# Performance work log

Measured on AMD Instinct MI355X. Metric: run time of the kernel, lower is better.

## Reference

```python
import jax, jax.numpy as jnp
import numpy as np

# --- low precision float format: exp=5, man=2, subnormals, nearest-even ---
EXP, MAN = 5, 2
BIAS = 2 ** (EXP - 1) - 1          # 15
EMIN = 1 - BIAS                     # -14 (min normal exponent; clamping here gives subnormals)
MAXV = (2.0 - 2.0 ** (-MAN)) * 2.0 ** BIAS


def _q(x):
    """Round x to nearest FP(exp=5, man=2) value (subnormals, clipped at max)."""
    ax = jnp.abs(x)
    e = jnp.floor(jnp.log2(jnp.where(ax > 0, ax, 1.0)))
    e = jnp.maximum(e, EMIN)
    scale = jnp.exp2(e - MAN)
    q = jnp.round(x / scale) * scale   # jnp.round = half-to-even
    q = jnp.clip(q, -MAXV, MAXV)
    return jnp.where(ax > 0, q, x).astype(x.dtype)


# Quantizer: forward quantize, straight-through (quantized) backward
@jax.custom_vjp
def fq(x):
    return _q(x)

def _fq_fwd(x):
    return _q(x), None

def _fq_bwd(_, g):
    return (_q(g),)

fq.defvjp(_fq_fwd, _fq_bwd)


def conv_valid(x, w):
    return jax.lax.conv_general_dilated(
        x, w, window_strides=(1, 1), padding='VALID',
        dimension_numbers=('NCHW', 'OIHW', 'NCHW'))


def qconv(x, w):
    # QConv2d: input_quant, weight_quant, conv, output_quant
    return fq(conv_valid(fq(x), fq(w)))


def qlinear(x, W, b):
    # QLinear: input_quant, weight_quant (weights + bias), matmul, output_quant
    return fq(fq(x) @ fq(W).T + fq(b))


def batchnorm(x, gamma, beta, eps=1e-5):
    # training-mode BatchNorm2d over (N,H,W) per channel
    m = x.mean(axis=(0, 2, 3), keepdims=True)
    v = x.var(axis=(0, 2, 3), keepdims=True)
    return (x - m) * jax.lax.rsqrt(v + eps) * gamma[None, :, None, None] + beta[None, :, None, None]


def maxpool2(x):
    return jax.lax.reduce_window(x, -jnp.inf, jax.lax.max,
                                 (1, 1, 2, 2), (1, 1, 2, 2), 'VALID')


def setup_inputs() -> dict:
    key = jax.random.key(0)
    ks = jax.random.split(key, 12)
    B = 8192
    inp = {
        'x':   jax.random.normal(ks[0], (B, 1, 32, 32), jnp.float32),
        'w1':  jax.random.normal(ks[1], (6, 1, 5, 5), jnp.float32) * 0.2,
        'g1':  jnp.ones((6,), jnp.float32),
        'be1': jnp.zeros((6,), jnp.float32),
        'w2':  jax.random.normal(ks[2], (16, 6, 5, 5), jnp.float32) * 0.1,
        'g2':  jnp.ones((16,), jnp.float32),
        'be2': jnp.zeros((16,), jnp.float32),
        'fw1': jax.random.normal(ks[3], (120, 400), jnp.float32) * 0.05,
        'fb1': jnp.zeros((120,), jnp.float32),
        'fw2': jax.random.normal(ks[4], (84, 120), jnp.float32) * 0.09,
        'fb2': jnp.zeros((84,), jnp.float32),
        'fw3': jax.random.normal(ks[5], (10, 84), jnp.float32) * 0.1,
        'fb3': jnp.zeros((10,), jnp.float32),
    }
    return inp


def reference(x, w1, g1, be1, w2, g2, be2, fw1, fb1, fw2, fb2, fw3, fb3):
    x = fq(x)                                   # act_error_quant
    x = qconv(x, w1)                            # conv1 (no bias)
    x = batchnorm(x, g1, be1)                   # bn1
    x = fq(x)                                   # act_error_quant
    x = maxpool2(jax.nn.relu(x))                # relu + 2x2 maxpool -> [B,6,14,14]
    x = qconv(x, w2)                            # conv2 -> [B,16,10,10]
    x = batchnorm(x, g2, be2)                   # bn2
    x = fq(x)
    x = maxpool2(jax.nn.relu(x))                # -> [B,16,5,5]
    x = x.reshape(x.shape[0], -1)               # [B,400]
    x = jax.nn.relu(qlinear(x, fw1, fb1))       # fc1
    x = jax.nn.relu(qlinear(x, fw2, fb2))       # fc2
    x = qlinear(x, fw3, fb3)                    # fc3 -> [B,10]
    return x
```

## Files before the change

kernel.cpp:

```cpp
#include <hip/hip_runtime.h>
#include <hip/hip_bf16.h>


#define BATCH 8192

__device__ __forceinline__ double fq_d(double x) {
    long long b = __double_as_longlong(x);
    long long ab = b & 0x7fffffffffffffffLL;
    if (ab == 0) return x;
    double q;
    if (ab >= 0x3F10000000000000LL) {
        long long r = b + 0x0001FFFFFFFFFFFFLL + ((b >> 50) & 1LL);
        r &= 0xFFFC000000000000LL;
        q = __longlong_as_double(r);
        q = fmin(fmax(q, -57344.0), 57344.0);
    } else {
        q = rint(x * 65536.0) * 1.52587890625e-05;
    }
    return q;
}

__device__ __forceinline__ unsigned short bfbits(double q) {
    __hip_bfloat16 h = __float2bfloat16((float)q);
    return *(unsigned short*)&h;
}

__global__ void kprep(const float* __restrict__ w1, const float* __restrict__ w2,
                      const float* __restrict__ fb1, const float* __restrict__ fb2,
                      const float* __restrict__ fb3, const float* __restrict__ fw1,
                      const float* __restrict__ fw2, const float* __restrict__ fw3,
                      float* __restrict__ qw1, float* __restrict__ qw2,
                      float* __restrict__ qfb1, float* __restrict__ qfb2,
                      float* __restrict__ qfb3, float* __restrict__ Wt1,
                      float* __restrict__ Wt2, float* __restrict__ Wt3) {
    int i = blockIdx.x * 256 + threadIdx.x;
    if (i < 150) { qw1[i] = (float)fq_d((double)w1[i]); return; }
    i -= 150;
    if (i < 2400) { qw2[i] = (float)fq_d((double)w2[i]); return; }
    i -= 2400;
    if (i < 120) { qfb1[i] = (float)fq_d((double)fb1[i]); return; }
    i -= 120;
    if (i < 84) { qfb2[i] = (float)fq_d((double)fb2[i]); return; }
    i -= 84;
    if (i < 10) { qfb3[i] = (float)fq_d((double)fb3[i]); return; }
    i -= 10;
    if (i < 51200) { int k = i / 128, o = i % 128;
        Wt1[i] = (o < 120) ? (float)fq_d((double)fw1[o * 400 + k]) : 0.0f; return; }
    i -= 51200;
    if (i < 15360) { int k = i / 128, o = i % 128;
        Wt2[i] = (o < 84) ? (float)fq_d((double)fw2[o * 120 + k]) : 0.0f; return; }
    i -= 15360;
    if (i < 1344) { int k = i / 16, o = i % 16;
        Wt3[i] = (o < 10) ? (float)fq_d((double)fw3[o * 84 + k]) : 0.0f; return; }
}
#define PREP_TOTAL (150 + 2400 + 120 + 84 + 10 + 51200 + 15360 + 1344)

__global__ __launch_bounds__(256) void kconv1(const float* __restrict__ x,
        const float* __restrict__ qw, __hip_bfloat16* __restrict__ c1,
        int nimg_total, double* __restrict__ st1) {
    __shared__ float sxf[3 * 1056];
    __shared__ double swd[152];
    __shared__ double sred[6][2];
    int t = threadIdx.x;
    int b0 = blockIdx.x * 3;
    int nimg = nimg_total - b0; if (nimg > 3) nimg = 3;
    for (int i = t; i < nimg * 1024; i += 256) {
        int img = i >> 10, idx = i & 1023;
        sxf[img * 1056 + (idx >> 5) * 33 + (idx & 31)] =
            (float)fq_d((double)x[(size_t)(b0 + img) * 1024 + idx]);
    }
    if (t < 150) swd[t] = (double)qw[t];
    if (t >= 192 && t < 204) ((double*)sred)[t - 192] = 0.0;
    __syncthreads();
    int ntask = nimg * 336;
    for (int task = t; task < ntask; task += 256) {
        int img = task / 336; int rr = task % 336;
        int co = rr / 56; int rem = rr % 56;
        int i0 = (rem >> 2) * 2;
        int j0 = (rem & 3) * 7;
        const float* xb = &sxf[img * 1056];
        const double* wp = &swd[co * 25];
        double a0[7], a1[7];
        #pragma unroll
        for (int j = 0; j < 7; ++j) { a0[j] = 0.0; a1[j] = 0.0; }
        double wr[5], wq[5];
        #pragma unroll
        for (int u = 0; u < 6; ++u) {
            const float* xr = &sxf[img * 1056 + (i0 + u) * 33 + j0];
            double xv[11];
            #pragma unroll
            for (int k = 0; k < 11; ++k) xv[k] = (double)xr[k];
            if (u < 5) {
                #pragma unroll
                for (int tt = 0; tt < 5; ++tt) wr[tt] = wp[u * 5 + tt];
                #pragma unroll
                for (int j = 0; j < 7; ++j)
                    a0[j] = fma(xv[j], wr[0], fma(xv[j+1], wr[1], fma(xv[j+2], wr[2],
                            fma(xv[j+3], wr[3], fma(xv[j+4], wr[4], a0[j])))));
            }
            if (u >= 1) {
                #pragma unroll
                for (int j = 0; j < 7; ++j)
                    a1[j] = fma(xv[j], wq[0], fma(xv[j+1], wq[1], fma(xv[j+2], wq[2],
                            fma(xv[j+3], wq[3], fma(xv[j+4], wq[4], a1[j])))));
            }
            #pragma unroll
            for (int tt = 0; tt < 5; ++tt) wq[tt] = wr[tt];
        }
        size_t base = ((size_t)(b0 + img) * 6 + co) * 784 + (size_t)i0 * 28 + j0;
        double s = 0.0, s2 = 0.0;
        #pragma unroll
        for (int j = 0; j < 7; ++j) {
            double q0 = fq_d(a0[j]), q1 = fq_d(a1[j]);
            ((unsigned short*)c1)[base + j]      = bfbits(q0);
            ((unsigned short*)c1)[base + 28 + j] = bfbits(q1);
            s += q0 + q1; s2 += q0 * q0 + q1 * q1;
        }
        atomicAdd(&sred[co][0], s);
        atomicAdd(&sred[co][1], s2);
    }
    __syncthreads();
    if (t < 12) atomicAdd(&st1[t * 32 + (blockIdx.x & 31)], ((double*)sred)[t]);
}

__global__ void kfinal(const double* __restrict__ st, double* __restrict__ mr,
                       int C, double N) {
    int c = threadIdx.x;
    if (c < C) {
        double s = 0.0, s2 = 0.0;
        for (int b = 0; b < 32; ++b) { s += st[c * 64 + b]; s2 += st[c * 64 + 32 + b]; }
        double m = s / N;
        double v = s2 / N - m * m;
        mr[2 * c] = m;
        mr[2 * c + 1] = 1.0 / sqrt(v + 1e-5);
    }
}

__global__ __launch_bounds__(256) void kpool1(const __hip_bfloat16* __restrict__ c1,
        const double* __restrict__ mr1, const float* __restrict__ g1,
        const float* __restrict__ be1, __hip_bfloat16* __restrict__ p1) {
    int idx = blockIdx.x * 256 + threadIdx.x;
    int pp = idx % 7;  int t1 = idx / 7;
    int ph = t1 % 14;  int t2 = t1 / 14;
    int c  = t2 % 6;   int b  = t2 / 6;
    double m = mr1[2 * c], r = mr1[2 * c + 1];
    double gg = (double)g1[c], bb = (double)be1[c];
    bool useMax = (r * gg) >= 0.0;
    const __hip_bfloat16* src = c1 + (((size_t)b * 6 + c) * 28 + 2 * ph) * 28 + 4 * pp;
    ushort4 u0 = *(const ushort4*)src;
    ushort4 u1 = *(const ushort4*)(src + 28);
    float f0 = __bfloat162float(*(__hip_bfloat16*)&u0.x), f1 = __bfloat162float(*(__hip_bfloat16*)&u0.y);
    float f2 = __bfloat162float(*(__hip_bfloat16*)&u0.z), f3 = __bfloat162float(*(__hip_bfloat16*)&u0.w);
    float f4 = __bfloat162float(*(__hip_bfloat16*)&u1.x), f5 = __bfloat162float(*(__hip_bfloat16*)&u1.y);
    float f6 = __bfloat162float(*(__hip_bfloat16*)&u1.z), f7 = __bfloat162float(*(__hip_bfloat16*)&u1.w);
    float va = useMax ? fmaxf(fmaxf(f0, f1), fmaxf(f4, f5))
                      : fminf(fminf(f0, f1), fminf(f4, f5));
    float vb = useMax ? fmaxf(fmaxf(f2, f3), fmaxf(f6, f7))
                      : fminf(fminf(f2, f3), fminf(f6, f7));
    double qa = fq_d((((double)va - m) * r) * gg + bb);
    double qb = fq_d((((double)vb - m) * r) * gg + bb);
    qa = fmax(qa, 0.0); qb = fmax(qb, 0.0);
    ushort2 pk; pk.x = bfbits(qa); pk.y = bfbits(qb);
    *(ushort2*)&p1[((size_t)b * 6 + c) * 196 + ph * 14 + 2 * pp] = pk;
}

__global__ __launch_bounds__(320) void kconv2(const __hip_bfloat16* __restrict__ p1,
        const float* __restrict__ qw, __hip_bfloat16* __restrict__ c2,
        double* __restrict__ st2) {
    __shared__ float sxf[4704];
    __shared__ float swf[2400];
    __shared__ double sred[16][2];
    int t = threadIdx.x;
    int b0 = blockIdx.x * 4;
    for (int i = t; i < 4704; i += 320) sxf[i] = __bfloat162float(p1[(size_t)b0 * 1176 + i]);
    for (int i = t; i < 2400; i += 320) swf[i] = qw[i];
    if (t < 32) ((double*)sred)[t] = 0.0;
    __syncthreads();
    int img = t / 80, r = t % 80;
    int co = r / 5, i0 = (r % 5) * 2;
    const float* xb = &sxf[img * 1176];
    const float* wb = &swf[co * 150];
    double a0[10], a1[10];
    #pragma unroll
    for (int j = 0; j < 10; ++j) { a0[j] = 0.0; a1[j] = 0.0; }
    double wr[5], wq[5];
    for (int ci = 0; ci < 6; ++ci) {
        #pragma unroll
        for (int u = 0; u < 6; ++u) {
            const float* xr = &xb[ci * 196 + (i0 + u) * 14];
            double xv[14];
            #pragma unroll
            for (int k = 0; k < 14; ++k) xv[k] = (double)xr[k];
            if (u < 5) {
                #pragma unroll
                for (int tt = 0; tt < 5; ++tt) wr[tt] = (double)wb[ci * 25 + u * 5 + tt];
                #pragma unroll
                for (int j = 0; j < 10; ++j)
                    a0[j] = fma(xv[j], wr[0], fma(xv[j+1], wr[1], fma(xv[j+2], wr[2],
                            fma(xv[j+3], wr[3], fma(xv[j+4], wr[4], a0[j])))));
            }
            if (u >= 1) {
                #pragma unroll
                for (int j = 0; j < 10; ++j)
                    a1[j] = fma(xv[j], wq[0], fma(xv[j+1], wq[1], fma(xv[j+2], wq[2],
                            fma(xv[j+3], wq[3], fma(xv[j+4], wq[4], a1[j])))));
            }
            #pragma unroll
            for (int tt = 0; tt < 5; ++tt) wq[tt] = wr[tt];
        }
    }
    size_t base = ((size_t)(b0 + img) * 16 + co) * 100 + (size_t)i0 * 10;
    double s = 0.0, s2 = 0.0;
    #pragma unroll
    for (int j = 0; j < 10; ++j) {
        double q0 = fq_d(a0[j]), q1 = fq_d(a1[j]);
        ((unsigned short*)c2)[base + j]      = bfbits(q0);
        ((unsigned short*)c2)[base + 10 + j] = bfbits(q1);
        s += q0 + q1; s2 += q0 * q0 + q1 * q1;
    }
    atomicAdd(&sred[co][0], s);
    atomicAdd(&sred[co][1], s2);
    __syncthreads();
    if (t < 32) atomicAdd(&st2[t * 32 + (blockIdx.x & 31)], ((double*)sred)[t]);
}

__global__ __launch_bounds__(256) void kfc1(const __hip_bfloat16* __restrict__ c2,
        const double* __restrict__ mr2, const float* __restrict__ g2,
        const float* __restrict__ be2, const float* __restrict__ Wt,
        const float* __restrict__ qb, __hip_bfloat16* __restrict__ outb) {
    constexpr int IN = 400, OUT = 120, OUTP = 128, ROWS = 8, BT = 16;
    __shared__ double sx[BT][IN];
    __shared__ double sbn[16][4];
    int t = threadIdx.x;
    int b0 = blockIdx.x * BT;
    if (t < 16) {
        sbn[t][0] = mr2[2 * t]; sbn[t][1] = mr2[2 * t + 1];
        sbn[t][2] = (double)g2[t]; sbn[t][3] = (double)be2[t];
    }
    __syncthreads();
    for (int i = t; i < BT * IN; i += 256) {
        int r = i / IN, k = i % IN;
        int c = k / 25, rem = k % 25;
        int ph = rem / 5, pw = rem % 5;
        const __hip_bfloat16* src = c2 + (((size_t)(b0 + r) * 16 + c) * 10 + 2 * ph) * 10 + 2 * pw;
        double m = sbn[c][0], rr = sbn[c][1], gg = sbn[c][2], bb = sbn[c][3];
        float f0 = __bfloat162float(src[0]),  f1 = __bfloat162float(src[1]);
        float f2 = __bfloat162float(src[10]), f3 = __bfloat162float(src[11]);
        bool useMax = (rr * gg) >= 0.0;
        float v = useMax ? fmaxf(fmaxf(f0, f1), fmaxf(f2, f3))
                         : fminf(fminf(f0, f1), fminf(f2, f3));
        double q = fq_d((((double)v - m) * rr) * gg + bb);
        sx[r][k] = fmax(q, 0.0);
    }
    __syncthreads();
    int o = t % OUTP;
    int g = t / OUTP;
    double acc[ROWS];
    double bias = (o < OUT) ? (double)qb[o] : 0.0;
    #pragma unroll
    for (int r = 0; r < ROWS; ++r) acc[r] = bias;
    #pragma unroll 4
    for (int k = 0; k < IN; ++k) {
        double w = (double)Wt[k * OUTP + o];
        #pragma unroll
        for (int r = 0; r < ROWS; ++r)
            acc[r] = fma(sx[g * ROWS + r][k], w, acc[r]);
    }
    if (o < OUT) {
        #pragma unroll
        for (int r = 0; r < ROWS; ++r) {
            double q = fq_d(acc[r]);
            if (q < 0.0) q = 0.0;
            outb[(size_t)(b0 + g * ROWS + r) * OUT + o] = __float2bfloat16((float)q);
        }
    }
}

template<int IN, int OUT, int OUTP, int ROWS>
__global__ __launch_bounds__(256) void kfc(const __hip_bfloat16* __restrict__ X,
        const float* __restrict__ Wt, const float* __restrict__ qb,
        __hip_bfloat16* __restrict__ outb, float* __restrict__ outf, int do_relu) {
    constexpr int GROUPS = 256 / OUTP;
    constexpr int BT = ROWS * GROUPS;
    __shared__ double sx[BT][IN];
    int t = threadIdx.x;
    int b0 = blockIdx.x * BT;
    for (int i = t; i < BT * IN; i += 256) {
        int r = i / IN, k = i % IN;
        sx[r][k] = (double)__bfloat162float(X[(size_t)(b0 + r) * IN + k]);
    }
    __syncthreads();
    int o = t % OUTP;
    int g = t / OUTP;
    double acc[ROWS];
    double bias = (o < OUT) ? (double)qb[o] : 0.0;
    #pragma unroll
    for (int r = 0; r < ROWS; ++r) acc[r] = bias;
    #pragma unroll 4
    for (int k = 0; k < IN; ++k) {
        double w = (double)Wt[k * OUTP + o];
        #pragma unroll
        for (int r = 0; r < ROWS; ++r)
            acc[r] = fma(sx[g * ROWS + r][k], w, acc[r]);
    }
    if (o < OUT) {
        #pragma unroll
        for (int r = 0; r < ROWS; ++r) {
            double q = fq_d(acc[r]);
            if (do_relu && q < 0.0) q = 0.0;
            size_t b = (size_t)(b0 + g * ROWS + r);
            if (outf) outf[b * OUT + o] = (float)q;
            else      outb[b * OUT + o] = __float2bfloat16((float)q);
        }
    }
}

extern "C" void kernel_launch(void* const* d_in, const int* in_sizes, int n_in,
                              void* d_out, int out_size, void* d_ws, size_t ws_size,
                              hipStream_t stream) {
    const float* x   = (const float*)d_in[0];
    const float* w1  = (const float*)d_in[1];
    const float* g1  = (const float*)d_in[2];
    const float* be1 = (const float*)d_in[3];
    const float* w2  = (const float*)d_in[4];
    const float* g2  = (const float*)d_in[5];
    const float* be2 = (const float*)d_in[6];
    const float* fw1 = (const float*)d_in[7];
    const float* fb1 = (const float*)d_in[8];
    const float* fw2 = (const float*)d_in[9];
    const float* fb2 = (const float*)d_in[10];
    const float* fw3 = (const float*)d_in[11];
    const float* fb3 = (const float*)d_in[12];

    char* ws = (char*)d_ws;
    double* stats1 = (double*)(ws + 0);
    double* stats2 = (double*)(ws + 3072);
    double* mr1    = (double*)(ws + 11264);
    double* mr2    = (double*)(ws + 11392);
    float* qw1  = (float*)(ws + 12288);
    float* qw2  = (float*)(ws + 13312);
    float* qfb1 = (float*)(ws + 23040);
    float* qfb2 = (float*)(ws + 23552);
    float* qfb3 = (float*)(ws + 24064);
    float* Wt1  = (float*)(ws + 24576);
    float* Wt2  = (float*)(ws + 229376);
    float* Wt3  = (float*)(ws + 290816);
    __hip_bfloat16* c1 = (__hip_bfloat16*)(ws + 303104);
    __hip_bfloat16* p1 = (__hip_bfloat16*)(ws + 77373440);
    __hip_bfloat16* c2 = (__hip_bfloat16*)(ws + 303104);
    __hip_bfloat16* a1 = (__hip_bfloat16*)(ws + 303104 + 26214400);
    __hip_bfloat16* a2 = (__hip_bfloat16*)(ws + 303104 + 28180480);

    hipMemsetAsync(ws, 0, 11264, stream);

    kprep<<<(PREP_TOTAL + 255) / 256, 256, 0, stream>>>(
        w1, w2, fb1, fb2, fb3, fw1, fw2, fw3,
        qw1, qw2, qfb1, qfb2, qfb3, Wt1, Wt2, Wt3);

    kconv1<<<(BATCH + 2) / 3, 256, 0, stream>>>(x, qw1, c1, BATCH, stats1);
    kfinal<<<1, 32, 0, stream>>>(stats1, mr1, 6, (double)BATCH * 784.0);
    kpool1<<<BATCH * 6 * 14 * 7 / 256, 256, 0, stream>>>(c1, mr1, g1, be1, p1);
    kconv2<<<BATCH / 4, 320, 0, stream>>>(p1, qw2, c2, stats2);
    kfinal<<<1, 32, 0, stream>>>(stats2, mr2, 16, (double)BATCH * 100.0);
    kfc1<<<BATCH / 16, 256, 0, stream>>>(c2, mr2, g2, be2, Wt1, qfb1, a1);
    kfc<120, 84, 128, 8><<<BATCH / 16, 256, 0, stream>>>(a1, Wt2, qfb2, a2, (float*)nullptr, 1);
    kfc<84, 10, 16, 1><<<BATCH / 16, 256, 0, stream>>>(a2, Wt3, qfb3, (__hip_bfloat16*)nullptr, (float*)d_out, 0);
}
```

Baseline: 436.4 us.

## Fuse fc2/fc3, fold BN2 finalize into fc1, use float quantizer

Merges the fc2 and fc3 kernels into one kernel that keeps the fc2 activations in shared memory, which removes the a2 round trip through global memory. It also drops the second kfinal launch by having each kfc1 block reduce the conv2 statistics itself, and halves the fc1 tile so twice as many blocks run. A float-precision quantizer replaces the double one for input and weight quantization. The trade-offs are redundant statistic reductions in every fc1 block and a possible rounding difference between the float and double quantizer paths.

```diff
diff --git a/kernel.cpp b/kernel.cpp
--- a/kernel.cpp
+++ b/kernel.cpp
@@ -20,6 +20,22 @@
     return q;
 }
 
+__device__ __forceinline__ float fq_f(float x) {
+    int b = __float_as_int(x);
+    int ab = b & 0x7fffffff;
+    if (ab == 0) return x;
+    float q;
+    if (ab >= 0x38800000) {
+        int r = b + 0x000FFFFF + ((b >> 21) & 1);
+        r &= 0xFFE00000;
+        q = __int_as_float(r);
+        q = fminf(fmaxf(q, -57344.0f), 57344.0f);
+    } else {
+        q = rintf(x * 65536.0f) * 1.52587890625e-05f;
+    }
+    return q;
+}
+
 __device__ __forceinline__ unsigned short bfbits(double q) {
     __hip_bfloat16 h = __float2bfloat16((float)q);
     return *(unsigned short*)&h;
@@ -34,24 +50,24 @@
                       float* __restrict__ qfb3, float* __restrict__ Wt1,
                       float* __restrict__ Wt2, float* __restrict__ Wt3) {
     int i = blockIdx.x * 256 + threadIdx.x;
-    if (i < 150) { qw1[i] = (float)fq_d((double)w1[i]); return; }
+    if (i < 150) { qw1[i] = fq_f(w1[i]); return; }
     i -= 150;
-    if (i < 2400) { qw2[i] = (float)fq_d((double)w2[i]); return; }
+    if (i < 2400) { qw2[i] = fq_f(w2[i]); return; }
     i -= 2400;
-    if (i < 120) { qfb1[i] = (float)fq_d((double)fb1[i]); return; }
+    if (i < 120) { qfb1[i] = fq_f(fb1[i]); return; }
     i -= 120;
-    if (i < 84) { qfb2[i] = (float)fq_d((double)fb2[i]); return; }
+    if (i < 84) { qfb2[i] = fq_f(fb2[i]); return; }
     i -= 84;
-    if (i < 10) { qfb3[i] = (float)fq_d((double)fb3[i]); return; }
+    if (i < 10) { qfb3[i] = fq_f(fb3[i]); return; }
     i -= 10;
     if (i < 51200) { int k = i / 128, o = i % 128;
-        Wt1[i] = (o < 120) ? (float)fq_d((double)fw1[o * 400 + k]) : 0.0f; return; }
+        Wt1[i] = (o < 120) ? fq_f(fw1[o * 400 + k]) : 0.0f; return; }
     i -= 51200;
     if (i < 15360) { int k = i / 128, o = i % 128;
-        Wt2[i] = (o < 84) ? (float)fq_d((double)fw2[o * 120 + k]) : 0.0f; return; }
+        Wt2[i] = (o < 84) ? fq_f(fw2[o * 120 + k]) : 0.0f; return; }
     i -= 15360;
     if (i < 1344) { int k = i / 16, o = i % 16;
-        Wt3[i] = (o < 10) ? (float)fq_d((double)fw3[o * 84 + k]) : 0.0f; return; }
+        Wt3[i] = (o < 10) ? fq_f(fw3[o * 84 + k]) : 0.0f; return; }
 }
 #define PREP_TOTAL (150 + 2400 + 120 + 84 + 10 + 51200 + 15360 + 1344)
 
@@ -67,7 +83,7 @@
     for (int i = t; i < nimg * 1024; i += 256) {
         int img = i >> 10, idx = i & 1023;
         sxf[img * 1056 + (idx >> 5) * 33 + (idx & 31)] =
-            (float)fq_d((double)x[(size_t)(b0 + img) * 1024 + idx]);
+            fq_f(x[(size_t)(b0 + img) * 1024 + idx]);
     }
     if (t < 150) swd[t] = (double)qw[t];
     if (t >= 192 && t < 204) ((double*)sred)[t - 192] = 0.0;
@@ -78,7 +94,6 @@
         int co = rr / 56; int rem = rr % 56;
         int i0 = (rem >> 2) * 2;
         int j0 = (rem & 3) * 7;
-        const float* xb = &sxf[img * 1056];
         const double* wp = &swd[co * 25];
         double a0[7], a1[7];
         #pragma unroll
@@ -225,16 +240,20 @@
 }
 
 __global__ __launch_bounds__(256) void kfc1(const __hip_bfloat16* __restrict__ c2,
-        const double* __restrict__ mr2, const float* __restrict__ g2,
+        const double* __restrict__ st2, const float* __restrict__ g2,
         const float* __restrict__ be2, const float* __restrict__ Wt,
         const float* __restrict__ qb, __hip_bfloat16* __restrict__ outb) {
-    constexpr int IN = 400, OUT = 120, OUTP = 128, ROWS = 8, BT = 16;
+    constexpr int IN = 400, OUT = 120, OUTP = 128, ROWS = 4, BT = 8;
     __shared__ double sx[BT][IN];
     __shared__ double sbn[16][4];
     int t = threadIdx.x;
     int b0 = blockIdx.x * BT;
     if (t < 16) {
-        sbn[t][0] = mr2[2 * t]; sbn[t][1] = mr2[2 * t + 1];
+        double s = 0.0, s2 = 0.0;
+        for (int b = 0; b < 32; ++b) { s += st2[t * 64 + b]; s2 += st2[t * 64 + 32 + b]; }
+        double m = s / (819200.0);
+        double v = s2 / (819200.0) - m * m;
+        sbn[t][0] = m; sbn[t][1] = 1.0 / sqrt(v + 1e-5);
         sbn[t][2] = (double)g2[t]; sbn[t][3] = (double)be2[t];
     }
     __syncthreads();
@@ -276,42 +295,49 @@
     }
 }
 
-template<int IN, int OUT, int OUTP, int ROWS>
-__global__ __launch_bounds__(256) void kfc(const __hip_bfloat16* __restrict__ X,
-        const float* __restrict__ Wt, const float* __restrict__ qb,
-        __hip_bfloat16* __restrict__ outb, float* __restrict__ outf, int do_relu) {
-    constexpr int GROUPS = 256 / OUTP;
-    constexpr int BT = ROWS * GROUPS;
-    __shared__ double sx[BT][IN];
+__global__ __launch_bounds__(256) void kfc23(const __hip_bfloat16* __restrict__ a1,
+        const float* __restrict__ Wt2, const float* __restrict__ qfb2,
+        const float* __restrict__ Wt3, const float* __restrict__ qfb3,
+        float* __restrict__ out) {
+    __shared__ double sx1[16][120];
+    __shared__ double s2[16][84];
     int t = threadIdx.x;
-    int b0 = blockIdx.x * BT;
-    for (int i = t; i < BT * IN; i += 256) {
-        int r = i / IN, k = i % IN;
-        sx[r][k] = (double)__bfloat162float(X[(size_t)(b0 + r) * IN + k]);
-    }
-    __syncthreads();
-    int o = t % OUTP;
-    int g = t / OUTP;
-    double acc[ROWS];
-    double bias = (o < OUT) ? (double)qb[o] : 0.0;
-    #pragma unroll
-    for (int r = 0; r < ROWS; ++r) acc[r] = bias;
-    #pragma unroll 4
-    for (int k = 0; k < IN; ++k) {
-        double w = (double)Wt[k * OUTP + o];
-        #pragma unroll
-        for (int r = 0; r < ROWS; ++r)
-            acc[r] = fma(sx[g * ROWS + r][k], w, acc[r]);
-    }
-    if (o < OUT) {
-        #pragma unroll
-        for (int r = 0; r < ROWS; ++r) {
-            double q = fq_d(acc[r]);
-            if (do_relu && q < 0.0) q = 0.0;
-            size_t b = (size_t)(b0 + g * ROWS + r);
-            if (outf) outf[b * OUT + o] = (float)q;
-            else      outb[b * OUT + o] = __float2bfloat16((float)q);
-        }
+    int b0 = blockIdx.x * 16;
+    for (int i = t; i < 16 * 120; i += 256) {
+        int r = i / 120, k = i % 120;
+        sx1[r][k] = (double)__bfloat162float(a1[(size_t)(b0 + r) * 120 + k]);
+    }
+    __syncthreads();
+    {
+        int o = t % 128, g = t / 128;
+        double acc[8];
+        double bias = (o < 84) ? (double)qfb2[o] : 0.0;
+        #pragma unroll
+        for (int r = 0; r < 8; ++r) acc[r] = bias;
+        #pragma unroll 4
+        for (int k = 0; k < 120; ++k) {
+            double w = (double)Wt2[k * 128 + o];
+            #pragma unroll
+            for (int r = 0; r < 8; ++r)
+                acc[r] = fma(sx1[g * 8 + r][k], w, acc[r]);
+        }
+        if (o < 84) {
+            #pragma unroll
+            for (int r = 0; r < 8; ++r) {
+                double q = fq_d(acc[r]);
+                s2[g * 8 + r][o] = fmax(q, 0.0);
+            }
+        }
+    }
+    __syncthreads();
+    {
+        int o = t % 16, g = t / 16;
+        double acc = (o < 10) ? (double)qfb3[o] : 0.0;
+        #pragma unroll 4
+        for (int k = 0; k < 84; ++k)
+            acc = fma(s2[g][k], (double)Wt3[k * 16 + o], acc);
+        if (o < 10)
+            out[(size_t)(b0 + g) * 10 + o] = (float)fq_d(acc);
     }
 }
 
@@ -336,7 +362,6 @@
     double* stats1 = (double*)(ws + 0);
     double* stats2 = (double*)(ws + 3072);
     double* mr1    = (double*)(ws + 11264);
-    double* mr2    = (double*)(ws + 11392);
     float* qw1  = (float*)(ws + 12288);
     float* qw2  = (float*)(ws + 13312);
     float* qfb1 = (float*)(ws + 23040);
@@ -349,7 +374,6 @@
     __hip_bfloat16* p1 = (__hip_bfloat16*)(ws + 77373440);
     __hip_bfloat16* c2 = (__hip_bfloat16*)(ws + 303104);
     __hip_bfloat16* a1 = (__hip_bfloat16*)(ws + 303104 + 26214400);
-    __hip_bfloat16* a2 = (__hip_bfloat16*)(ws + 303104 + 28180480);
 
     hipMemsetAsync(ws, 0, 11264, stream);
 
@@ -361,8 +385,6 @@
     kfinal<<<1, 32, 0, stream>>>(stats1, mr1, 6, (double)BATCH * 784.0);
     kpool1<<<BATCH * 6 * 14 * 7 / 256, 256, 0, stream>>>(c1, mr1, g1, be1, p1);
     kconv2<<<BATCH / 4, 320, 0, stream>>>(p1, qw2, c2, stats2);
-    kfinal<<<1, 32, 0, stream>>>(stats2, mr2, 16, (double)BATCH * 100.0);
-    kfc1<<<BATCH / 16, 256, 0, stream>>>(c2, mr2, g2, be2, Wt1, qfb1, a1);
-    kfc<120, 84, 128, 8><<<BATCH / 16, 256, 0, stream>>>(a1, Wt2, qfb2, a2, (float*)nullptr, 1);
-    kfc<84, 10, 16, 1><<<BATCH / 16, 256, 0, stream>>>(a2, Wt3, qfb3, (__hip_bfloat16*)nullptr, (float*)d_out, 0);
-}
+    kfc1<<<BATCH / 8, 256, 0, stream>>>(c2, stats2, g2, be2, Wt1, qfb1, a1);
+    kfc23<<<BATCH / 16, 256, 0, stream>>>(a1, Wt2, qfb2, Wt3, qfb3, (float*)d_out);
+}
```

Result: faster. 410.5 us (-5.9%).
